# Performance work log

Measured on AMD Instinct MI355X. Metric: run time of the kernel, lower is better.

Reference implementation:

```python
import jax, jax.numpy as jnp
import numpy as np

T, B, S, E, H = 64, 64, 128, 512, 1024  # tgt_len, batch, src_len, emb, hidden


def setup_inputs() -> dict:
    key = jax.random.key(0)
    ks = jax.random.split(key, 14)
    s = 0.02  # weight init scale
    f32 = jnp.float32
    return {
        "inp": jax.random.normal(ks[0], (T, B, E), f32),
        "context": jax.random.normal(ks[1], (S, B, H), f32),
        "h0": jax.random.normal(ks[2], (2, B, H), f32) * 0.1,
        "c0": jax.random.normal(ks[3], (2, B, H), f32) * 0.1,
        # layer 0 LSTMCell: input = emb + input-feed = E + H
        "W_ih0": jax.random.normal(ks[4], (4 * H, E + H), f32) * s,
        "b_ih0": jnp.zeros((4 * H,), f32),
        "W_hh0": jax.random.normal(ks[5], (4 * H, H), f32) * s,
        "b_hh0": jnp.zeros((4 * H,), f32),
        # layer 1 LSTMCell: input = H
        "W_ih1": jax.random.normal(ks[6], (4 * H, H), f32) * s,
        "b_ih1": jnp.zeros((4 * H,), f32),
        "W_hh1": jax.random.normal(ks[7], (4 * H, H), f32) * s,
        "b_hh1": jnp.zeros((4 * H,), f32),
        # global attention (general): linear_in W_a (H,H), linear_out (H, 2H) no bias
        "W_a": jax.random.normal(ks[8], (H, H), f32) * s,
        "W_out": jax.random.normal(ks[9], (H, 2 * H), f32) * s,
    }


def _lstm_cell(x, h, c, W_ih, b_ih, W_hh, b_hh):
    # PyTorch gate order: i, f, g, o
    g = x @ W_ih.T + b_ih + h @ W_hh.T + b_hh
    i, f, gg, o = jnp.split(g, 4, axis=-1)
    c2 = jax.nn.sigmoid(f) * c + jax.nn.sigmoid(i) * jnp.tanh(gg)
    h2 = jax.nn.sigmoid(o) * jnp.tanh(c2)
    return h2, c2


def reference(inp, context, h0, c0, W_ih0, b_ih0, W_hh0, b_hh0,
              W_ih1, b_ih1, W_hh1, b_hh1, W_a, W_out):
    ctx_bt = jnp.transpose(context, (1, 0, 2))          # (B, S, H)
    # score(h, s) = h . (ctx_s @ W_a)  (== (h @ W_a.T) . ctx_s)
    ctx_p = jnp.einsum('bsk,kd->bsd', ctx_bt, W_a)      # (B, S, H)

    def step(carry, emb_t):
        h, c, out = carry                                # h,c: (2,B,H); out: (B,H)
        x = jnp.concatenate([emb_t, out], axis=1)        # (B, E+H) input feed
        h0n, c0n = _lstm_cell(x, h[0], c[0], W_ih0, b_ih0, W_hh0, b_hh0)
        h1n, c1n = _lstm_cell(h0n, h[1], c[1], W_ih1, b_ih1, W_hh1, b_hh1)
        score = jnp.einsum('bh,bsh->bs', h1n, ctx_p)     # (B, S)
        align = jax.nn.softmax(score, axis=-1)
        cvec = jnp.einsum('bs,bsh->bh', align, ctx_bt)   # (B, H)
        attn_h = jnp.tanh(jnp.concatenate([cvec, h1n], axis=1) @ W_out.T)
        hn = jnp.stack([h0n, h1n])
        cn = jnp.stack([c0n, c1n])
        return (hn, cn, attn_h), (attn_h, align)

    out0 = jnp.zeros((context.shape[1], W_a.shape[0]), context.dtype)
    (hF, cF, _), (outs, attns) = jax.lax.scan(step, (h0, c0, out0), inp)
    # outs: (T, B, H); hF, cF: (2, B, H); attns: (T, B, S)
    return outs, hF, cF, attns
```

## Files before the change

kernel.cpp:

```cpp
#include <hip/hip_runtime.h>

#define T_ 64
#define B_ 64
#define S_ 128
#define E_ 512
#define H_ 1024
#define BH (B_ * H_)

#define W0ROW (E_ + 2 * H_ + 8)
#define W1ROW (2 * H_ + 8)
#define SMEM_BYTES ((16 * W0ROW + 16 * W1ROW) * 2)

typedef __attribute__((ext_vector_type(8))) short short8;
typedef __attribute__((ext_vector_type(4))) short short4v;
typedef __attribute__((ext_vector_type(4))) float f32x4;

static __device__ __forceinline__ float bf2f(ushort u) {
  union { float f; unsigned u; } x; x.u = ((unsigned)u) << 16; return x.f;
}
static __device__ __forceinline__ ushort f2bf(float f) {
  union { float f; unsigned u; } x; x.f = f;
  unsigned r = 0x7FFFu + ((x.u >> 16) & 1u);
  return (ushort)((x.u + r) >> 16);
}
static __device__ __forceinline__ float sigm(float x) {
  return 1.f / (1.f + expf(-x));
}

static __device__ __forceinline__ void st32_dev(unsigned* p, unsigned v) {
  __hip_atomic_store(p, v, __ATOMIC_RELAXED, __HIP_MEMORY_SCOPE_AGENT);
}
static __device__ __forceinline__ unsigned ld32_dev(const unsigned* p) {
  return __hip_atomic_load(p, __ATOMIC_RELAXED, __HIP_MEMORY_SCOPE_AGENT);
}
static __device__ __forceinline__ void stf_dev(float* p, float v) {
  union { float f; unsigned u; } x; x.f = v;
  st32_dev((unsigned*)p, x.u);
}

__global__ __launch_bounds__(256) void k_cvt(const float* __restrict__ src,
                                             ushort* __restrict__ dst, int n4) {
  int i = blockIdx.x * 256 + threadIdx.x;
  if (i >= n4) return;
  f32x4 v = ((const f32x4*)src)[i];
  short4v o;
  o[0] = (short)f2bf(v[0]); o[1] = (short)f2bf(v[1]);
  o[2] = (short)f2bf(v[2]); o[3] = (short)f2bf(v[3]);
  ((short4v*)dst)[i] = o;
}

__global__ __launch_bounds__(256) void k_cvtT(const float* __restrict__ src,
                                              ushort* __restrict__ dst) {
  __shared__ ushort tile[32][33];
  const int bx = blockIdx.x & 31;
  const int by = blockIdx.x >> 5;
  const int lx = threadIdx.x & 31, ly = threadIdx.x >> 5;
#pragma unroll
  for (int i = 0; i < 32; i += 8)
    tile[ly + i][lx] = f2bf(src[(size_t)(by * 32 + ly + i) * H_ + bx * 32 + lx]);
  __syncthreads();
#pragma unroll
  for (int i = 0; i < 32; i += 8)
    dst[(size_t)(bx * 32 + ly + i) * H_ + by * 32 + lx] = tile[lx][ly + i];
}

__global__ __launch_bounds__(256) void k_ctxp(const ushort* __restrict__ ctx,
                                              const ushort* __restrict__ WaT,
                                              ushort* __restrict__ ctxp) {
  const int tid = threadIdx.x;
  const int wave = tid >> 6, lane = tid & 63;
  const int quad = lane >> 4, l16 = lane & 15;
  const int m0 = blockIdx.x * 64 + wave * 16;
  const int n0 = blockIdx.y * 64;
  const ushort* ar = ctx + (size_t)(m0 + l16) * H_;
  const int koff = quad * 8;
  f32x4 acc[4] = {};
  for (int k0 = 0; k0 < H_; k0 += 32) {
    int kk = k0 + koff;
    short8 a = *(const short8*)(ar + kk);
#pragma unroll
    for (int nt = 0; nt < 4; ++nt) {
      short8 b = *(const short8*)(WaT + (size_t)(n0 + nt * 16 + l16) * H_ + kk);
      acc[nt] = __builtin_amdgcn_mfma_f32_16x16x32_bf16(a, b, acc[nt], 0, 0, 0);
    }
  }
#pragma unroll
  for (int nt = 0; nt < 4; ++nt)
#pragma unroll
    for (int r = 0; r < 4; ++r)
      ctxp[(size_t)(m0 + quad * 4 + r) * H_ + n0 + nt * 16 + l16] =
          f2bf(acc[nt][r]);
}

__global__ __launch_bounds__(256) void k_ctxo(const ushort* __restrict__ ctx,
                                              const ushort* __restrict__ Wout,
                                              ushort* __restrict__ ctxo) {
  const int tid = threadIdx.x;
  const int wave = tid >> 6, lane = tid & 63;
  const int quad = lane >> 4, l16 = lane & 15;
  const int m0 = blockIdx.x * 64 + wave * 16;
  const int n0 = blockIdx.y * 64;
  const ushort* ar = ctx + (size_t)(m0 + l16) * H_;
  const int koff = quad * 8;
  f32x4 acc[4] = {};
  for (int k0 = 0; k0 < H_; k0 += 32) {
    int kk = k0 + koff;
    short8 a = *(const short8*)(ar + kk);
#pragma unroll
    for (int nt = 0; nt < 4; ++nt) {
      short8 b = *(const short8*)(Wout +
                                  (size_t)(n0 + nt * 16 + l16) * (2 * H_) + kk);
      acc[nt] = __builtin_amdgcn_mfma_f32_16x16x32_bf16(a, b, acc[nt], 0, 0, 0);
    }
  }
#pragma unroll
  for (int nt = 0; nt < 4; ++nt)
#pragma unroll
    for (int r = 0; r < 4; ++r)
      ctxo[(size_t)(m0 + quad * 4 + r) * H_ + n0 + nt * 16 + l16] =
          f2bf(acc[nt][r]);
}

__global__ __launch_bounds__(256) void k_init(const float* __restrict__ h0in,
                                              ushort* __restrict__ h0b,
                                              ushort* __restrict__ h1b,
                                              ushort* __restrict__ fdb,
                                              unsigned* __restrict__ flags) {
  int i = blockIdx.x * 256 + threadIdx.x;
  h0b[i] = f2bf(h0in[i]);
  h1b[i] = f2bf(h0in[BH + i]);
  fdb[i] = 0;
  if (blockIdx.x == 0) flags[threadIdx.x * 16] = 0;
}

static __device__ __forceinline__ void grid_bar(unsigned* flags, unsigned gen) {
  __syncthreads();
  if (blockIdx.x == 0) {
    const int tid = threadIdx.x;
    if (tid > 0 && tid < 256) {
      while (ld32_dev(&flags[tid * 16]) < gen) __builtin_amdgcn_s_sleep(4);
    }
    __syncthreads();
    if (tid == 0) st32_dev(&flags[0], gen);
    __syncthreads();
  } else {
    if (threadIdx.x == 0) {
      st32_dev(&flags[blockIdx.x * 16], gen);
      while (ld32_dev(&flags[0]) < gen) __builtin_amdgcn_s_sleep(4);
    }
    __syncthreads();
  }
  asm volatile("" ::: "memory");
}

struct FusedP {
  const ushort* inp;
  const ushort* Wih0; const ushort* Whh0;
  const ushort* Wih1; const ushort* Whh1;
  const ushort* Wout;
  const ushort* ctxp;
  const ushort* ctxo;
  const float* bih0; const float* bhh0;
  const float* bih1; const float* bhh1;
  const float* c0in;
  ushort* h0b;
  ushort* h1b;
  ushort* fdb;
  float* psb;
  float* gemmb;
  float* outs; float* hF; float* cF; float* attns;
  unsigned* flags;
};

#define ST(w, r, c) ub[(w) * 272 + (r) * 17 + (c)]
#define RED(w, i)   ub[(w) * 256 + (i)]

__global__ __launch_bounds__(1024, 1) void k_fused(FusedP p) {
  extern __shared__ ushort wlds[];
  ushort* w0 = wlds;
  ushort* w1 = wlds + 16 * W0ROW;
  __shared__ float ub[2176];
  __shared__ float al[S_];
  const int blk = blockIdx.x;
  const int tid = threadIdx.x;
  const int wave = tid >> 6, lane = tid & 63;
  const int wg = wave & 3;
  const int kh = wave >> 2;
  const int quad = lane >> 4, l16 = lane & 15;
  const int j0 = blk * 4;

  for (int idx = tid; idx < 16 * 192; idx += 1024) {
    int r = idx / 192, c = (idx % 192) * 8;
    int n = (r >> 2) * H_ + j0 + (r & 3);
    *(short8*)(w0 + r * W0ROW + c) =
        *(const short8*)(p.Wih0 + (size_t)n * (E_ + H_) + c);
  }
  for (int idx = tid; idx < 16 * 128; idx += 1024) {
    int r = idx / 128, c = (idx % 128) * 8;
    int n = (r >> 2) * H_ + j0 + (r & 3);
    *(short8*)(w0 + r * W0ROW + (E_ + H_) + c) =
        *(const short8*)(p.Whh0 + (size_t)n * H_ + c);
  }
  for (int idx = tid; idx < 16 * 128; idx += 1024) {
    int r = idx / 128, c = (idx % 128) * 8;
    int n = (r >> 2) * H_ + j0 + (r & 3);
    *(short8*)(w1 + r * W1ROW + c) =
        *(const short8*)(p.Wih1 + (size_t)n * H_ + c);
  }
  for (int idx = tid; idx < 16 * 128; idx += 1024) {
    int r = idx / 128, c = (idx % 128) * 8;
    int n = (r >> 2) * H_ + j0 + (r & 3);
    *(short8*)(w1 + r * W1ROW + H_ + c) =
        *(const short8*)(p.Whh1 + (size_t)n * H_ + c);
  }
  __syncthreads();

  const int own_b = tid >> 2;
  const int own_jl = tid & 3;
  const int own_j = j0 + own_jl;
  const int own_idx = own_b * H_ + own_j;
  float c0reg = 0.f, c1reg = 0.f;
  float b0i = 0.f, b0f = 0.f, b0g = 0.f, b0o = 0.f;
  float b1i = 0.f, b1f = 0.f, b1g = 0.f, b1o = 0.f;
  if (tid < 256) {
    c0reg = p.c0in[own_idx];
    c1reg = p.c0in[BH + own_idx];
    b0i = p.bih0[own_j]          + p.bhh0[own_j];
    b0f = p.bih0[H_ + own_j]     + p.bhh0[H_ + own_j];
    b0g = p.bih0[2 * H_ + own_j] + p.bhh0[2 * H_ + own_j];
    b0o = p.bih0[3 * H_ + own_j] + p.bhh0[3 * H_ + own_j];
    b1i = p.bih1[own_j]          + p.bhh1[own_j];
    b1f = p.bih1[H_ + own_j]     + p.bhh1[H_ + own_j];
    b1g = p.bih1[2 * H_ + own_j] + p.bhh1[2 * H_ + own_j];
    b1o = p.bih1[3 * H_ + own_j] + p.bhh1[3 * H_ + own_j];
  }

  const ushort* w0r = w0 + l16 * W0ROW;
  const ushort* w1r = w1 + l16 * W1ROW;
  const int koff = quad * 8;

  const int b3 = blk >> 2, dq = blk & 3;
  const int d0 = dq * 256;

  short4v cp[8], co[8];
#pragma unroll
  for (int i = 0; i < 8; ++i) {
    const int s = wave * 8 + i;
    cp[i] = *(const short4v*)(p.ctxp + ((size_t)s * B_ + b3) * H_ +
                              d0 + lane * 4);
    co[i] = *(const short4v*)(p.ctxo + ((size_t)s * B_ + b3) * H_ +
                              d0 + lane * 4);
  }

  unsigned gen = 0;

  for (int t = 0; t < T_; ++t) {
    const ushort* h0prev = p.h0b + (size_t)t * BH;
    ushort* h0new       = p.h0b + (size_t)(t + 1) * BH;
    const ushort* h1prev = p.h1b + (size_t)t * BH;
    ushort* h1new       = p.h1b + (size_t)(t + 1) * BH;
    const ushort* feedr  = p.fdb + (size_t)t * BH;
    ushort* feedw       = p.fdb + (size_t)(t + 1) * BH;
    float* pst          = p.psb + (size_t)t * B_ * S_ * 4;
    float* gemm_t       = p.gemmb + (size_t)t * BH;
    const int last = (t == T_ - 1);

    {
      const int arow = 16 * wg + l16;
      const ushort* er = p.inp + ((size_t)t * B_ + arow) * E_;
      const ushort* fr = feedr + (size_t)arow * H_;
      const ushort* hr = h0prev + (size_t)arow * H_;
      const int kbase = kh * 640;
      f32x4 acc = {};
#pragma unroll
      for (int k0 = 0; k0 < 640; k0 += 32) {
        int kk = kbase + k0 + koff;
        short8 a;
        if (kk < E_)            a = *(const short8*)(er + kk);
        else if (kk < E_ + H_)  a = *(const short8*)(fr + (kk - E_));
        else                    a = *(const short8*)(hr + (kk - E_ - H_));
        short8 b = *(const short8*)(w0r + kk);
        acc = __builtin_amdgcn_mfma_f32_16x16x32_bf16(a, b, acc, 0, 0, 0);
      }
      if (kh >= 2) {
#pragma unroll
        for (int r = 0; r < 4; ++r) ST(wave - 8, quad * 4 + r, l16) = acc[r];
      }
      __syncthreads();
      if (kh < 2) {
#pragma unroll
        for (int r = 0; r < 4; ++r) {
          float s = ST(wave, quad * 4 + r, l16) + acc[r];
          ST(wave, quad * 4 + r, l16) = s;
        }
      }
      __syncthreads();
      if (tid < 256) {
        const int w = own_b >> 4, bl = own_b & 15;
        float gi = ST(w, bl, 0 + own_jl)  + ST(w + 4, bl, 0 + own_jl)  + b0i;
        float gf = ST(w, bl, 4 + own_jl)  + ST(w + 4, bl, 4 + own_jl)  + b0f;
        float gg = ST(w, bl, 8 + own_jl)  + ST(w + 4, bl, 8 + own_jl)  + b0g;
        float go = ST(w, bl, 12 + own_jl) + ST(w + 4, bl, 12 + own_jl) + b0o;
        float cn = sigm(gf) * c0reg + sigm(gi) * tanhf(gg);
        float hn = sigm(go) * tanhf(cn);
        c0reg = cn;
        if (last) { p.hF[own_idx] = hn; p.cF[own_idx] = cn; }
        unsigned u = f2bf(hn);
        unsigned up = __shfl_down(u, 1);
        if (!(own_jl & 1))
          st32_dev((unsigned*)h0new + own_b * (H_ / 2) + blk * 2 + (own_jl >> 1),
                   u | (up << 16));
      }
    }
    grid_bar(p.flags, ++gen);

    {
      const int arow = 16 * wg + l16;
      const ushort* xr = h0new + (size_t)arow * H_;
      const ushort* hr = h1prev + (size_t)arow * H_;
      const int kbase = kh * 512;
      f32x4 acc = {};
#pragma unroll
      for (int k0 = 0; k0 < 512; k0 += 32) {
        int kk = kbase + k0 + koff;
        short8 a = (kk < H_) ? *(const short8*)(xr + kk)
                             : *(const short8*)(hr + (kk - H_));
        short8 b = *(const short8*)(w1r + kk);
        acc = __builtin_amdgcn_mfma_f32_16x16x32_bf16(a, b, acc, 0, 0, 0);
      }
      if (kh >= 2) {
#pragma unroll
        for (int r = 0; r < 4; ++r) ST(wave - 8, quad * 4 + r, l16) = acc[r];
      }
      __syncthreads();
      if (kh < 2) {
#pragma unroll
        for (int r = 0; r < 4; ++r) {
          float s = ST(wave, quad * 4 + r, l16) + acc[r];
          ST(wave, quad * 4 + r, l16) = s;
        }
      }
      __syncthreads();
      if (tid < 256) {
        const int w = own_b >> 4, bl = own_b & 15;
        float gi = ST(w, bl, 0 + own_jl)  + ST(w + 4, bl, 0 + own_jl)  + b1i;
        float gf = ST(w, bl, 4 + own_jl)  + ST(w + 4, bl, 4 + own_jl)  + b1f;
        float gg = ST(w, bl, 8 + own_jl)  + ST(w + 4, bl, 8 + own_jl)  + b1g;
        float go = ST(w, bl, 12 + own_jl) + ST(w + 4, bl, 12 + own_jl) + b1o;
        float cn = sigm(gf) * c1reg + sigm(gi) * tanhf(gg);
        float hn = sigm(go) * tanhf(cn);
        c1reg = cn;
        if (last) { p.hF[BH + own_idx] = hn; p.cF[BH + own_idx] = cn; }
        unsigned u = f2bf(hn);
        unsigned up = __shfl_down(u, 1);
        if (!(own_jl & 1))
          st32_dev((unsigned*)h1new + own_b * (H_ / 2) + blk * 2 + (own_jl >> 1),
                   u | (up << 16));
      }
    }
    grid_bar(p.flags, ++gen);

    {
      short4v qv = *(const short4v*)(h1new + (size_t)b3 * H_ + d0 + lane * 4);
      float q0 = bf2f((ushort)qv[0]), q1 = bf2f((ushort)qv[1]);
      float q2 = bf2f((ushort)qv[2]), q3 = bf2f((ushort)qv[3]);
#pragma unroll
      for (int i = 0; i < 8; ++i) {
        const int s = wave * 8 + i;
        float pr = bf2f((ushort)cp[i][0]) * q0 + bf2f((ushort)cp[i][1]) * q1 +
                   bf2f((ushort)cp[i][2]) * q2 + bf2f((ushort)cp[i][3]) * q3;
#pragma unroll
        for (int off = 32; off; off >>= 1) pr += __shfl_down(pr, off);
        if (lane == 0) stf_dev(pst + (b3 * S_ + s) * 4 + dq, pr);
      }
      if (blk < 64) {
        const int pj0 = blk * 16;
        const int arow = 16 * wg + l16;
        const ushort* hr2 = h1new + (size_t)arow * H_;
        const ushort* wr = p.Wout + (size_t)(pj0 + l16) * (2 * H_) + H_;
        const int kbase = kh * 256;
        f32x4 acc = {};
#pragma unroll
        for (int k0 = 0; k0 < 256; k0 += 32) {
          int kk = kbase + k0 + koff;
          acc = __builtin_amdgcn_mfma_f32_16x16x32_bf16(
              *(const short8*)(hr2 + kk), *(const short8*)(wr + kk), acc,
              0, 0, 0);
        }
        if (kh >= 2) {
#pragma unroll
          for (int r = 0; r < 4; ++r) ST(wave - 8, quad * 4 + r, l16) = acc[r];
        }
        __syncthreads();
        if (kh < 2) {
#pragma unroll
          for (int r = 0; r < 4; ++r) {
            float s = ST(wave, quad * 4 + r, l16) + acc[r];
            ST(wave, quad * 4 + r, l16) = s;
          }
        }
        __syncthreads();
        {
          const int b = tid >> 4;
          const int jl = tid & 15;
          const int w = b >> 4, bl = b & 15;
          stf_dev(gemm_t + b * H_ + pj0 + jl,
                  ST(w, bl, jl) + ST(w + 4, bl, jl));
        }
      }
    }
    grid_bar(p.flags, ++gen);

    {
      if (tid < S_) {
        f32x4 ps = *(const f32x4*)(pst + (b3 * S_ + tid) * 4);
        al[tid] = ps[0] + ps[1] + ps[2] + ps[3];
      }
      __syncthreads();
      if (wave == 0) {
        float m = fmaxf(al[lane], al[lane + 64]);
#pragma unroll
        for (int off = 32; off; off >>= 1) m = fmaxf(m, __shfl_down(m, off));
        m = __shfl(m, 0);
        float e0 = expf(al[lane] - m), e1 = expf(al[lane + 64] - m);
        float s2 = e0 + e1;
#pragma unroll
        for (int off = 32; off; off >>= 1) s2 += __shfl_down(s2, off);
        s2 = __shfl(s2, 0);
        float inv = 1.f / s2;
        al[lane] = e0 * inv;
        al[lane + 64] = e1 * inv;
      }
      __syncthreads();
      if (dq == 0 && tid < S_)
        p.attns[((size_t)t * B_ + b3) * S_ + tid] = al[tid];
      float a0 = 0.f, a1 = 0.f, a2 = 0.f, a3 = 0.f;
#pragma unroll
      for (int i = 0; i < 8; ++i) {
        const int s = wave * 8 + i;
        float w = al[s];
        a0 += w * bf2f((ushort)co[i][0]);
        a1 += w * bf2f((ushort)co[i][1]);
        a2 += w * bf2f((ushort)co[i][2]);
        a3 += w * bf2f((ushort)co[i][3]);
      }
      __syncthreads();
      if (wave >= 8) {
        RED(wave - 8, lane * 4 + 0) = a0;
        RED(wave - 8, lane * 4 + 1) = a1;
        RED(wave - 8, lane * 4 + 2) = a2;
        RED(wave - 8, lane * 4 + 3) = a3;
      }
      __syncthreads();
      if (wave < 8) {
        RED(wave, lane * 4 + 0) += a0;
        RED(wave, lane * 4 + 1) += a1;
        RED(wave, lane * 4 + 2) += a2;
        RED(wave, lane * 4 + 3) += a3;
      }
      __syncthreads();
      if (tid < 256) {
        const int jj = tid;
        float val = 0.f;
#pragma unroll
        for (int w = 0; w < 8; ++w) val += RED(w, jj);
        val += gemm_t[b3 * H_ + d0 + jj];
        float v = tanhf(val);
        p.outs[(size_t)t * B_ * H_ + b3 * H_ + d0 + jj] = v;
        unsigned u = f2bf(v);
        unsigned up = __shfl_down(u, 1);
        if (!(jj & 1))
          st32_dev((unsigned*)feedw + (b3 * H_ + d0 + jj) / 2, u | (up << 16));
      }
    }
    grid_bar(p.flags, ++gen);
  }
}

extern "C" void kernel_launch(void* const* d_in, const int* in_sizes, int n_in,
                              void* d_out, int out_size, void* d_ws, size_t ws_size,
                              hipStream_t stream) {
  const float* inpf  = (const float*)d_in[0];
  const float* ctxf  = (const float*)d_in[1];
  const float* h0in  = (const float*)d_in[2];
  const float* c0in  = (const float*)d_in[3];
  const float* Wih0f = (const float*)d_in[4];
  const float* bih0  = (const float*)d_in[5];
  const float* Whh0f = (const float*)d_in[6];
  const float* bhh0  = (const float*)d_in[7];
  const float* Wih1f = (const float*)d_in[8];
  const float* bih1  = (const float*)d_in[9];
  const float* Whh1f = (const float*)d_in[10];
  const float* bhh1  = (const float*)d_in[11];
  const float* Waf   = (const float*)d_in[12];
  const float* Woutf = (const float*)d_in[13];

  float* out = (float*)d_out;
  float* outs  = out;
  float* hF    = out + (size_t)T_ * B_ * H_;
  float* cF    = hF + 2 * BH;
  float* attns = cF + 2 * BH;

  char* p = (char*)d_ws;
  auto take = [&](size_t bytes) -> char* {
    char* q = p;
    p += (bytes + 255) & ~(size_t)255;
    return q;
  };
  ushort* h0b  = (ushort*)take((size_t)(T_ + 1) * BH * 2);
  ushort* h1b  = (ushort*)take((size_t)(T_ + 1) * BH * 2);
  ushort* fdb  = (ushort*)take((size_t)(T_ + 1) * BH * 2);
  float* psb   = (float*)take((size_t)T_ * B_ * S_ * 4 * 4);
  float* gemmb = (float*)take((size_t)T_ * BH * 4);
  unsigned* flags = (unsigned*)take(256 * 16 * sizeof(unsigned));
  ushort* WaT  = (ushort*)take((size_t)H_ * H_ * 2);
  ushort* ctxp = (ushort*)take((size_t)S_ * B_ * H_ * 2);
  ushort* ctxo = (ushort*)take((size_t)S_ * B_ * H_ * 2);

  struct { const float* src; int n; } cv[7] = {
    {Wih0f, 4 * H_ * (E_ + H_)}, {Whh0f, 4 * H_ * H_},
    {Wih1f, 4 * H_ * H_},        {Whh1f, 4 * H_ * H_},
    {Woutf, 2 * H_ * H_},
    {inpf,  T_ * B_ * E_},       {ctxf,  S_ * B_ * H_},
  };
  ushort* cb[7];
  for (int i = 0; i < 7; ++i) {
    cb[i] = (ushort*)take((size_t)cv[i].n * 2);
    int n4 = cv[i].n / 4;
    k_cvt<<<(n4 + 255) / 256, 256, 0, stream>>>(cv[i].src, cb[i], n4);
  }
  const ushort *Wih0 = cb[0], *Whh0 = cb[1], *Wih1 = cb[2], *Whh1 = cb[3],
               *Wout = cb[4], *inp = cb[5], *ctx = cb[6];

  k_cvtT<<<(H_ / 32) * (H_ / 32), 256, 0, stream>>>(Waf, WaT);
  k_ctxp<<<dim3((S_ * B_) / 64, H_ / 64), 256, 0, stream>>>(ctx, WaT, ctxp);
  k_ctxo<<<dim3((S_ * B_) / 64, H_ / 64), 256, 0, stream>>>(ctx, Wout, ctxo);
  k_init<<<BH / 256, 256, 0, stream>>>(h0in, h0b, h1b, fdb, flags);

  static int smem_set = 0;
  if (!smem_set) {
    hipFuncSetAttribute((const void*)k_fused,
                        hipFuncAttributeMaxDynamicSharedMemorySize, SMEM_BYTES);
    smem_set = 1;
  }

  FusedP fp;
  fp.inp = inp; fp.Wih0 = Wih0; fp.Whh0 = Whh0; fp.Wih1 = Wih1; fp.Whh1 = Whh1;
  fp.Wout = Wout; fp.ctxp = ctxp; fp.ctxo = ctxo;
  fp.bih0 = bih0; fp.bhh0 = bhh0; fp.bih1 = bih1; fp.bhh1 = bhh1;
  fp.c0in = c0in;
  fp.h0b = h0b; fp.h1b = h1b; fp.fdb = fdb; fp.psb = psb; fp.gemmb = gemmb;
  fp.outs = outs; fp.hF = hF; fp.cF = cF; fp.attns = attns;
  fp.flags = flags;
  void* kargs[] = {(void*)&fp};
  hipLaunchCooperativeKernel(k_fused, dim3(256), dim3(1024), kargs,
                             (unsigned)SMEM_BYTES, stream);
}
```

Baseline: 2.865 ms.

## Precompute next step's layer-0 input and hidden GEMM parts inside split barrier

Splits the grid barrier after layer 1 into arrive and wait halves. Between them, each block computes the next timestep's layer-0 gate partial products from the embedding and the previous layer-0 hidden state, which are already available. Only the input-feed part of the layer-0 GEMM is left on the critical path after attention. The aim is to hide barrier latency behind useful MFMA work, at the cost of keeping an extra accumulator live in registers across the loop body.

```diff
diff --git a/kernel.cpp b/kernel.cpp
--- a/kernel.cpp
+++ b/kernel.cpp
@@ -146,6 +146,29 @@
   } else {
     if (threadIdx.x == 0) {
       st32_dev(&flags[blockIdx.x * 16], gen);
+      while (ld32_dev(&flags[0]) < gen) __builtin_amdgcn_s_sleep(4);
+    }
+    __syncthreads();
+  }
+  asm volatile("" ::: "memory");
+}
+static __device__ __forceinline__ void bar_arrive(unsigned* flags,
+                                                  unsigned gen) {
+  __syncthreads();
+  if (blockIdx.x != 0 && threadIdx.x == 0)
+    st32_dev(&flags[blockIdx.x * 16], gen);
+}
+static __device__ __forceinline__ void bar_wait(unsigned* flags, unsigned gen) {
+  if (blockIdx.x == 0) {
+    const int tid = threadIdx.x;
+    if (tid > 0 && tid < 256) {
+      while (ld32_dev(&flags[tid * 16]) < gen) __builtin_amdgcn_s_sleep(4);
+    }
+    __syncthreads();
+    if (tid == 0) st32_dev(&flags[0], gen);
+    __syncthreads();
+  } else {
+    if (threadIdx.x == 0) {
       while (ld32_dev(&flags[0]) < gen) __builtin_amdgcn_s_sleep(4);
     }
     __syncthreads();
@@ -238,6 +261,7 @@
   const ushort* w0r = w0 + l16 * W0ROW;
   const ushort* w1r = w1 + l16 * W1ROW;
   const int koff = quad * 8;
+  const int arow = 16 * wg + l16;
 
   const int b3 = blk >> 2, dq = blk & 3;
   const int d0 = dq * 256;
@@ -252,10 +276,31 @@
                               d0 + lane * 4);
   }
 
+  auto pre_p1 = [&](int tt) -> f32x4 {
+    const ushort* er = p.inp + ((size_t)tt * B_ + arow) * E_;
+    const ushort* hr = p.h0b + (size_t)tt * BH + (size_t)arow * H_;
+    f32x4 a = {};
+#pragma unroll
+    for (int k0 = 0; k0 < 128; k0 += 32) {
+      int kk = kh * 128 + k0 + koff;
+      a = __builtin_amdgcn_mfma_f32_16x16x32_bf16(
+          *(const short8*)(er + kk), *(const short8*)(w0r + kk), a, 0, 0, 0);
+    }
+#pragma unroll
+    for (int k0 = 0; k0 < 256; k0 += 32) {
+      int kk = 1536 + kh * 256 + k0 + koff;
+      a = __builtin_amdgcn_mfma_f32_16x16x32_bf16(
+          *(const short8*)(hr + (kk - 1536)), *(const short8*)(w0r + kk), a,
+          0, 0, 0);
+    }
+    return a;
+  };
+
+  f32x4 acc_p1 = pre_p1(0);
+
   unsigned gen = 0;
 
   for (int t = 0; t < T_; ++t) {
-    const ushort* h0prev = p.h0b + (size_t)t * BH;
     ushort* h0new       = p.h0b + (size_t)(t + 1) * BH;
     const ushort* h1prev = p.h1b + (size_t)t * BH;
     ushort* h1new       = p.h1b + (size_t)(t + 1) * BH;
@@ -266,21 +311,14 @@
     const int last = (t == T_ - 1);
 
     {
-      const int arow = 16 * wg + l16;
-      const ushort* er = p.inp + ((size_t)t * B_ + arow) * E_;
       const ushort* fr = feedr + (size_t)arow * H_;
-      const ushort* hr = h0prev + (size_t)arow * H_;
-      const int kbase = kh * 640;
-      f32x4 acc = {};
-#pragma unroll
-      for (int k0 = 0; k0 < 640; k0 += 32) {
-        int kk = kbase + k0 + koff;
-        short8 a;
-        if (kk < E_)            a = *(const short8*)(er + kk);
-        else if (kk < E_ + H_)  a = *(const short8*)(fr + (kk - E_));
-        else                    a = *(const short8*)(hr + (kk - E_ - H_));
-        short8 b = *(const short8*)(w0r + kk);
-        acc = __builtin_amdgcn_mfma_f32_16x16x32_bf16(a, b, acc, 0, 0, 0);
+      f32x4 acc = acc_p1;
+#pragma unroll
+      for (int k0 = 0; k0 < 256; k0 += 32) {
+        int kk = 512 + kh * 256 + k0 + koff;
+        acc = __builtin_amdgcn_mfma_f32_16x16x32_bf16(
+            *(const short8*)(fr + (kk - 512)), *(const short8*)(w0r + kk), acc,
+            0, 0, 0);
       }
       if (kh >= 2) {
 #pragma unroll
@@ -315,7 +353,6 @@
     grid_bar(p.flags, ++gen);
 
     {
-      const int arow = 16 * wg + l16;
       const ushort* xr = h0new + (size_t)arow * H_;
       const ushort* hr = h1prev + (size_t)arow * H_;
       const int kbase = kh * 512;
@@ -358,7 +395,9 @@
                    u | (up << 16));
       }
     }
-    grid_bar(p.flags, ++gen);
+    bar_arrive(p.flags, ++gen);
+    if (!last) acc_p1 = pre_p1(t + 1);
+    bar_wait(p.flags, gen);
 
     {
       short4v qv = *(const short4v*)(h1new + (size_t)b3 * H_ + d0 + lane * 4);
@@ -375,7 +414,6 @@
       }
       if (blk < 64) {
         const int pj0 = blk * 16;
-        const int arow = 16 * wg + l16;
         const ushort* hr2 = h1new + (size_t)arow * H_;
         const ushort* wr = p.Wout + (size_t)(pj0 + l16) * (2 * H_) + H_;
         const int kbase = kh * 256;
```

Result: no change. 2.896 ms (+1.1%).
